# Kernel tuning notes

Measured on AMD Instinct MI355X. Metric: run time of the kernel, lower is better.

## Reference

```python
import jax, jax.numpy as jnp
import numpy as np

EMBED = 1024
HEADS = 16
HEAD_DIM = EMBED // HEADS


def setup_inputs() -> dict:
    key = jax.random.key(0)
    ks = jax.random.split(key, 5)
    s = 1.0 / np.sqrt(EMBED)
    x = jax.random.normal(ks[0], (2, 2048, EMBED), dtype=jnp.float32)
    W_qkv = jax.random.uniform(ks[1], (EMBED, 3 * EMBED), dtype=jnp.float32, minval=-s, maxval=s)
    b_qkv = jax.random.uniform(ks[2], (3 * EMBED,), dtype=jnp.float32, minval=-s, maxval=s)
    W_out = jax.random.uniform(ks[3], (EMBED, EMBED), dtype=jnp.float32, minval=-s, maxval=s)
    b_out = jax.random.uniform(ks[4], (EMBED,), dtype=jnp.float32, minval=-s, maxval=s)
    return {"x": x, "W_qkv": W_qkv, "b_qkv": b_qkv, "W_out": W_out, "b_out": b_out}


def reference(x, W_qkv, b_qkv, W_out, b_out):
    B, S, E = x.shape
    qkv = x @ W_qkv + b_qkv                              # [B,S,3E]
    qkv = qkv.reshape(B, S, 3, HEADS, HEAD_DIM)
    q, k, v = qkv[:, :, 0], qkv[:, :, 1], qkv[:, :, 2]   # [B,S,H,D]
    q = q.transpose(0, 2, 1, 3)                          # [B,H,S,D]
    k = k.transpose(0, 2, 1, 3)
    v = v.transpose(0, 2, 1, 3)
    scale = 1.0 / np.sqrt(HEAD_DIM).astype(np.float32)
    scores = jnp.einsum('bhqd,bhkd->bhqk', q, k) * scale  # [B,H,S,S]
    causal = jnp.tril(jnp.ones((S, S), dtype=bool))
    scores = jnp.where(causal, scores, jnp.float32(-jnp.inf))
    attn = jax.nn.softmax(scores, axis=-1)
    out = jnp.einsum('bhqk,bhkd->bhqd', attn, v)          # [B,H,S,D]
    out = out.transpose(0, 2, 1, 3).reshape(B, S, E)
    return out @ W_out + b_out
```

## Files before the change

kernel.cpp:

```cpp
#include <hip/hip_runtime.h>
#include <hip/hip_bf16.h>
#include <math.h>

typedef __bf16 bf16;
typedef bf16 bf16x4 __attribute__((ext_vector_type(4)));
typedef bf16 bf16x8 __attribute__((ext_vector_type(8)));
typedef float f32x4 __attribute__((ext_vector_type(4)));
typedef float f32x16 __attribute__((ext_vector_type(16)));
typedef unsigned int uint;

#define EMB 1024
#define SEQ 2048
#define BATCH 2
#define NH 16
#define HD 64

#define SCALE2 0.18033688011112042f

__device__ __forceinline__ void glds16(const void* g, void* l) {
  __builtin_amdgcn_global_load_lds(
      (__attribute__((address_space(1))) void*)g,
      (__attribute__((address_space(3))) void*)l, 16, 0, 0);
}

__device__ __forceinline__ uint cvtpk(float lo, float hi) {
  uint r;
  asm("v_cvt_pk_bf16_f32 %0, %1, %2" : "=v"(r) : "v"(lo), "v"(hi));
  return r;
}
__device__ __forceinline__ void plswap(uint& a, uint& b) {
  asm("v_permlane32_swap_b32 %0, %1" : "+v"(a), "+v"(b));
}

__global__ __launch_bounds__(256) void cvt_f32_bf16(const float* __restrict__ in,
                                                    bf16* __restrict__ out, int n) {
  int i = (blockIdx.x * 256 + threadIdx.x) * 4;
  if (i < n) {
    float4 v = *reinterpret_cast<const float4*>(in + i);
    out[i + 0] = (bf16)v.x;
    out[i + 1] = (bf16)v.y;
    out[i + 2] = (bf16)v.z;
    out[i + 3] = (bf16)v.w;
  }
}

__global__ __launch_bounds__(256) void transpose_cvt(const float* __restrict__ in,
                                                     bf16* __restrict__ out,
                                                     int R, int C) {
  __shared__ float tile[32][33];
  int c0 = blockIdx.x * 32, r0 = blockIdx.y * 32;
  int tx = threadIdx.x, ty = threadIdx.y;
#pragma unroll
  for (int i = 0; i < 32; i += 8)
    tile[ty + i][tx] = in[(size_t)(r0 + ty + i) * C + c0 + tx];
  __syncthreads();
#pragma unroll
  for (int i = 0; i < 32; i += 8)
    out[(size_t)(c0 + ty + i) * R + r0 + tx] = (bf16)tile[tx][ty + i];
}

#define BM 128
#define BN 128
#define BK 32

__global__ __launch_bounds__(256) void gemm_bf16(
    const bf16* __restrict__ A, const bf16* __restrict__ Bt,
    const float* __restrict__ bias, int M, int N, int K,
    float* __restrict__ outF,
    bf16* __restrict__ outQ, bf16* __restrict__ outK, bf16* __restrict__ outVt,
    int mode) {
  __shared__ bf16 Alds[BM][BK];
  __shared__ bf16 Blds[BN][BK];

  const int t = threadIdx.x;
  const int lane = t & 63;
  const int w = t >> 6;
  const int wr = w >> 1, wc = w & 1;
  const int lg = lane >> 4, lr = lane & 15;
  const int m0 = blockIdx.y * BM;
  const int n0 = blockIdx.x * BN;

  const int c0 = w * 64 + lane;
  const int c1 = 256 + w * 64 + lane;
  const int r0 = c0 >> 2, ch0 = c0 & 3;
  const int r1 = c1 >> 2, ch1 = c1 & 3;

  f32x4 acc[4][4] = {};

  for (int k0 = 0; k0 < K; k0 += BK) {
    __syncthreads();
    glds16(A + (size_t)(m0 + r0) * K + k0 + ch0 * 8, &Alds[0][0] + c0 * 8);
    glds16(A + (size_t)(m0 + r1) * K + k0 + ch1 * 8, &Alds[0][0] + c1 * 8);
    glds16(Bt + (size_t)(n0 + r0) * K + k0 + ch0 * 8, &Blds[0][0] + c0 * 8);
    glds16(Bt + (size_t)(n0 + r1) * K + k0 + ch1 * 8, &Blds[0][0] + c1 * 8);
    __syncthreads();

    bf16x8 af[4], bfr[4];
#pragma unroll
    for (int i = 0; i < 4; ++i)
      af[i] = *reinterpret_cast<const bf16x8*>(&Alds[wr * 64 + i * 16 + lr][lg * 8]);
#pragma unroll
    for (int j = 0; j < 4; ++j)
      bfr[j] = *reinterpret_cast<const bf16x8*>(&Blds[wc * 64 + j * 16 + lr][lg * 8]);
#pragma unroll
    for (int i = 0; i < 4; ++i)
#pragma unroll
      for (int j = 0; j < 4; ++j)
        acc[i][j] = __builtin_amdgcn_mfma_f32_16x16x32_bf16(af[i], bfr[j], acc[i][j], 0, 0, 0);
  }

#pragma unroll
  for (int j = 0; j < 4; ++j) {
    const int n = n0 + wc * 64 + j * 16 + lr;
    const float bi = bias[n];
#pragma unroll
    for (int i = 0; i < 4; ++i) {
      const int mb = m0 + wr * 64 + i * 16 + lg * 4;
      if (mode == 0) {
#pragma unroll
        for (int r = 0; r < 4; ++r)
          outF[(size_t)(mb + r) * N + n] = acc[i][j][r] + bi;
      } else {
        const int which = n >> 10, rem = n & 1023;
        const int hh = rem >> 6, d = rem & 63;
        const int bb = mb >> 11, ss = mb & 2047;
        if (which == 2) {
          bf16x4 pv;
#pragma unroll
          for (int r = 0; r < 4; ++r) pv[r] = (bf16)(acc[i][j][r] + bi);
          *reinterpret_cast<bf16x4*>(
              outVt + (((size_t)bb * NH + hh) * HD + d) * SEQ + ss) = pv;
        } else if (which == 0) {
          bf16* dst = outQ + (((size_t)bb * NH + hh) * SEQ + ss) * HD + d;
#pragma unroll
          for (int r = 0; r < 4; ++r)
            dst[(size_t)r * HD] = (bf16)((acc[i][j][r] + bi) * SCALE2);
        } else {
          bf16* dst = outK + (((size_t)bb * NH + hh) * SEQ + ss) * HD + d;
#pragma unroll
          for (int r = 0; r < 4; ++r) dst[(size_t)r * HD] = (bf16)(acc[i][j][r] + bi);
        }
      }
    }
  }
}


#define STAGE(kt_, buf_)                                                       \
  {                                                                            \
    const int kb_ = (kt_) << 6;                                                \
    _Pragma("unroll")                                                          \
    for (int j = 0; j < 4; ++j) {                                              \
      const int g = (j * 2 + w) * 64 + lane;                                   \
      const int row = g >> 3, cc = g & 7;                                      \
      const int pc = (cc ^ (row & 7)) << 3;                                    \
      glds16(Kb + headoff + (size_t)(kb_ + row) * HD + pc, &Kl[buf_][g * 8]);  \
      glds16(Vt + headoff + (size_t)row * SEQ + kb_ + pc, &Vl[buf_][g * 8]);   \
    }                                                                          \
  }

__global__ __launch_bounds__(128, 2) void attn_fwd(
    const bf16* __restrict__ Qb, const bf16* __restrict__ Kb,
    const bf16* __restrict__ Vt, bf16* __restrict__ Ob) {
  __shared__ bf16 Kl[2][64 * 64];
  __shared__ bf16 Vl[2][64 * 64];

  const int t = threadIdx.x;
  const int lane = t & 63;
  const int w = t >> 6;
  const int l31 = lane & 31;
  const int hi = lane >> 5;
  const int hi8 = hi << 3;
  const int swz = l31 & 7;

  const int id = blockIdx.x;
  const int qsup = 31 - (id >> 5);
  const int bh = id & 31;
  const int h = bh & 15, b = bh >> 4;
  const size_t headoff = ((size_t)b * NH + h) * SEQ * HD;
  const int qrow = qsup * 64 + w * 32 + l31;

  bf16x8 qf[4];
  {
    const bf16* qr = Qb + headoff + (size_t)qrow * HD + hi8;
#pragma unroll
    for (int d = 0; d < 4; ++d) qf[d] = *reinterpret_cast<const bf16x8*>(qr + d * 16);
  }

  f32x16 accO0 = {}, accO1 = {};
  float m = -1e30f, lsum = 0.f;
  const int nkt = qsup + 1;

  STAGE(0, 0);
  __syncthreads();

  for (int kt = 0; kt < nkt; ++kt) {
    const int cur = kt & 1;
    if (kt + 1 < nkt) STAGE(kt + 1, cur ^ 1);

    const int kb = kt << 6;
    f32x16 s0 = {}, s1 = {};
    __builtin_amdgcn_s_setprio(1);
#pragma unroll
    for (int dd = 0; dd < 4; ++dd) {
      const int pc = ((dd * 2 + hi) ^ swz) << 3;
      bf16x8 kf0 = *reinterpret_cast<const bf16x8*>(&Kl[cur][l31 * 64 + pc]);
      bf16x8 kf1 = *reinterpret_cast<const bf16x8*>(&Kl[cur][(l31 + 32) * 64 + pc]);
      s0 = __builtin_amdgcn_mfma_f32_32x32x16_bf16(kf0, qf[dd], s0, 0, 0, 0);
      s1 = __builtin_amdgcn_mfma_f32_32x32x16_bf16(kf1, qf[dd], s1, 0, 0, 0);
    }
    __builtin_amdgcn_s_setprio(0);
    if (kt == nkt - 1) {
      const int kq = kb + hi * 4 - qrow;
#pragma unroll
      for (int r = 0; r < 16; ++r) {
        const int off = (r & 3) + 8 * (r >> 2);
        if (kq + off > 0) s0[r] = -1e30f;
        if (kq + off + 32 > 0) s1[r] = -1e30f;
      }
    }
    float pm[16];
#pragma unroll
    for (int r = 0; r < 16; ++r) pm[r] = fmaxf(s0[r], s1[r]);
#pragma unroll
    for (int st = 8; st > 0; st >>= 1)
#pragma unroll
      for (int r = 0; r < st; ++r) pm[r] = fmaxf(pm[r], pm[r + st]);
    const float tm = fmaxf(pm[0], __shfl_xor(pm[0], 32));
    if (!__all(tm <= m + 8.f)) {
      const float newm = fmaxf(m, tm);
      const float corr = __builtin_amdgcn_exp2f(m - newm);
      m = newm;
      lsum *= corr;
      accO0 *= corr;
      accO1 *= corr;
    }
#pragma unroll
    for (int r = 0; r < 16; ++r) {
      s0[r] = __builtin_amdgcn_exp2f(s0[r] - m);
      s1[r] = __builtin_amdgcn_exp2f(s1[r] - m);
    }
    float ps[16];
#pragma unroll
    for (int r = 0; r < 16; ++r) ps[r] = s0[r] + s1[r];
#pragma unroll
    for (int st = 8; st > 0; st >>= 1)
#pragma unroll
      for (int r = 0; r < st; ++r) ps[r] += ps[r + st];
    lsum += ps[0] + __shfl_xor(ps[0], 32);
    uint wv[16];
    wv[0]  = cvtpk(s0[0],  s0[1]);  wv[1]  = cvtpk(s0[2],  s0[3]);
    wv[2]  = cvtpk(s0[4],  s0[5]);  wv[3]  = cvtpk(s0[6],  s0[7]);
    wv[4]  = cvtpk(s0[8],  s0[9]);  wv[5]  = cvtpk(s0[10], s0[11]);
    wv[6]  = cvtpk(s0[12], s0[13]); wv[7]  = cvtpk(s0[14], s0[15]);
    wv[8]  = cvtpk(s1[0],  s1[1]);  wv[9]  = cvtpk(s1[2],  s1[3]);
    wv[10] = cvtpk(s1[4],  s1[5]);  wv[11] = cvtpk(s1[6],  s1[7]);
    wv[12] = cvtpk(s1[8],  s1[9]);  wv[13] = cvtpk(s1[10], s1[11]);
    wv[14] = cvtpk(s1[12], s1[13]); wv[15] = cvtpk(s1[14], s1[15]);
    plswap(wv[0], wv[2]);   plswap(wv[1], wv[3]);
    plswap(wv[4], wv[6]);   plswap(wv[5], wv[7]);
    plswap(wv[8], wv[10]);  plswap(wv[9], wv[11]);
    plswap(wv[12], wv[14]); plswap(wv[13], wv[15]);
    __builtin_amdgcn_s_setprio(1);
#pragma unroll
    for (int ks = 0; ks < 4; ++ks) {
      uint4 u = make_uint4(wv[ks * 4], wv[ks * 4 + 1], wv[ks * 4 + 2], wv[ks * 4 + 3]);
      bf16x8 pf = *reinterpret_cast<bf16x8*>(&u);
      const int pc = ((ks * 2 + hi) ^ swz) << 3;
      bf16x8 vf0 = *reinterpret_cast<const bf16x8*>(&Vl[cur][l31 * 64 + pc]);
      bf16x8 vf1 = *reinterpret_cast<const bf16x8*>(&Vl[cur][(l31 + 32) * 64 + pc]);
      accO0 = __builtin_amdgcn_mfma_f32_32x32x16_bf16(vf0, pf, accO0, 0, 0, 0);
      accO1 = __builtin_amdgcn_mfma_f32_32x32x16_bf16(vf1, pf, accO1, 0, 0, 0);
    }
    __builtin_amdgcn_s_setprio(0);
    __syncthreads();
  }

  const float inv = 1.0f / lsum;
  bf16* orow = Ob + ((size_t)b * SEQ + qrow) * EMB + h * HD + hi * 4;
#pragma unroll
  for (int rq = 0; rq < 4; ++rq) {
    bf16x4 o0, o1;
#pragma unroll
    for (int i = 0; i < 4; ++i) {
      o0[i] = (bf16)(accO0[rq * 4 + i] * inv);
      o1[i] = (bf16)(accO1[rq * 4 + i] * inv);
    }
    *reinterpret_cast<bf16x4*>(orow + rq * 8) = o0;
    *reinterpret_cast<bf16x4*>(orow + 32 + rq * 8) = o1;
  }
}

extern "C" void kernel_launch(void* const* d_in, const int* in_sizes, int n_in,
                              void* d_out, int out_size, void* d_ws, size_t ws_size,
                              hipStream_t stream) {
  const float* x    = (const float*)d_in[0];
  const float* Wqkv = (const float*)d_in[1];
  const float* bqkv = (const float*)d_in[2];
  const float* Wout = (const float*)d_in[3];
  const float* bout = (const float*)d_in[4];
  float* out = (float*)d_out;

  char* ws = (char*)d_ws;
  bf16* xb     = (bf16*)(ws);
  bf16* wqkvt  = (bf16*)(ws + 8388608);
  bf16* woutt  = (bf16*)(ws + 14680064);
  bf16* Qb     = (bf16*)(ws + 16777216);
  bf16* Kb     = (bf16*)(ws + 25165824);
  bf16* Vtb    = (bf16*)(ws + 33554432);
  bf16* attnb  = (bf16*)(ws + 41943040);

  const int n1 = 4096 * 1024;
  cvt_f32_bf16<<<(n1 / 4 + 255) / 256, 256, 0, stream>>>(x, xb, n1);
  dim3 tb(32, 8);
  transpose_cvt<<<dim3(3072 / 32, 1024 / 32), tb, 0, stream>>>(Wqkv, wqkvt, 1024, 3072);
  transpose_cvt<<<dim3(1024 / 32, 1024 / 32), tb, 0, stream>>>(Wout, woutt, 1024, 1024);

  dim3 g1(3072 / BN, 4096 / BM);
  gemm_bf16<<<g1, 256, 0, stream>>>(xb, wqkvt, bqkv, 4096, 3072, 1024,
                                    nullptr, Qb, Kb, Vtb, 1);

  attn_fwd<<<1024, 128, 0, stream>>>(Qb, Kb, Vtb, attnb);

  dim3 g2(1024 / BN, 4096 / BM);
  gemm_bf16<<<g2, 256, 0, stream>>>(attnb, woutt, bout, 4096, 1024, 1024,
                                    out, nullptr, nullptr, nullptr, 0);
}
```

Measured before the change: 129.4 us.

## Enlarge attention tiles to 128 queries and 128 keys per block

The attention kernel moves from 64-query blocks of two waves to 128-query blocks of four waves. Each pipeline stage now brings in a 128-key K/V tile with a wider swizzle, so each staged tile serves twice as many query rows and block count and loop trips are halved. On the diagonal tile, QK and PV MFMAs for fully masked 32-key sub-tiles are skipped, and the block order is rearranged for the new 16 query blocks. The cost is many more live score registers (four 32x32 accumulators) and twice the LDS per block, which may reduce occupancy or cause spills.

```diff
diff --git a/kernel.cpp b/kernel.cpp
--- a/kernel.cpp
+++ b/kernel.cpp
@@ -148,22 +148,35 @@
 
 #define STAGE(kt_, buf_)                                                       \
   {                                                                            \
-    const int kb_ = (kt_) << 6;                                                \
+    const int kb_ = (kt_) << 7;                                                \
     _Pragma("unroll")                                                          \
     for (int j = 0; j < 4; ++j) {                                              \
-      const int g = (j * 2 + w) * 64 + lane;                                   \
-      const int row = g >> 3, cc = g & 7;                                      \
-      const int pc = (cc ^ (row & 7)) << 3;                                    \
-      glds16(Kb + headoff + (size_t)(kb_ + row) * HD + pc, &Kl[buf_][g * 8]);  \
-      glds16(Vt + headoff + (size_t)row * SEQ + kb_ + pc, &Vl[buf_][g * 8]);   \
+      const int g = j * 256 + t;                                               \
+      const int rowK = g >> 3, ccK = g & 7;                                    \
+      const int pcK = ((ccK ^ (rowK & 7)) << 3);                               \
+      glds16(Kb + headoff + (size_t)(kb_ + rowK) * HD + pcK, &Kl[buf_][g * 8]);\
+      const int rowV = g >> 4, ccV = g & 15;                                   \
+      const int pcV = ((ccV ^ (rowV & 15)) << 3);                              \
+      glds16(Vt + headoff + (size_t)rowV * SEQ + kb_ + pcV, &Vl[buf_][g * 8]); \
     }                                                                          \
   }
 
-__global__ __launch_bounds__(128, 2) void attn_fwd(
+#define QK_ACC(SX, X)                                                          \
+  if (!diag || (X) <= w) {                                                     \
+    _Pragma("unroll")                                                          \
+    for (int dd = 0; dd < 4; ++dd) {                                           \
+      const int pcK = (((dd * 2 + hi) ^ swzK) << 3);                           \
+      bf16x8 kf = *reinterpret_cast<const bf16x8*>(                            \
+          &Kl[cur][((X) * 32 + l31) * 64 + pcK]);                              \
+      SX = __builtin_amdgcn_mfma_f32_32x32x16_bf16(kf, qf[dd], SX, 0, 0, 0);   \
+    }                                                                          \
+  }
+
+__global__ __launch_bounds__(256, 2) void attn_fwd(
     const bf16* __restrict__ Qb, const bf16* __restrict__ Kb,
     const bf16* __restrict__ Vt, bf16* __restrict__ Ob) {
-  __shared__ bf16 Kl[2][64 * 64];
-  __shared__ bf16 Vl[2][64 * 64];
+  __shared__ bf16 Kl[2][128 * 64];
+  __shared__ bf16 Vl[2][64 * 128];
 
   const int t = threadIdx.x;
   const int lane = t & 63;
@@ -171,14 +184,15 @@
   const int l31 = lane & 31;
   const int hi = lane >> 5;
   const int hi8 = hi << 3;
-  const int swz = l31 & 7;
+  const int swzK = l31 & 7;
+  const int swzV = l31 & 15;
 
   const int id = blockIdx.x;
-  const int qsup = 31 - (id >> 5);
+  const int qb = (id < 256) ? (15 - (id >> 5)) : ((id - 256) >> 5);
   const int bh = id & 31;
   const int h = bh & 15, b = bh >> 4;
   const size_t headoff = ((size_t)b * NH + h) * SEQ * HD;
-  const int qrow = qsup * 64 + w * 32 + l31;
+  const int qrow = qb * 128 + w * 32 + l31;
 
   bf16x8 qf[4];
   {
@@ -189,7 +203,7 @@
 
   f32x16 accO0 = {}, accO1 = {};
   float m = -1e30f, lsum = 0.f;
-  const int nkt = qsup + 1;
+  const int nkt = qb + 1;
 
   STAGE(0, 0);
   __syncthreads();
@@ -198,30 +212,30 @@
     const int cur = kt & 1;
     if (kt + 1 < nkt) STAGE(kt + 1, cur ^ 1);
 
-    const int kb = kt << 6;
-    f32x16 s0 = {}, s1 = {};
+    const int kb = kt << 7;
+    const bool diag = (kt == nkt - 1);
+    f32x16 s0 = {}, s1 = {}, s2 = {}, s3 = {};
     __builtin_amdgcn_s_setprio(1);
-#pragma unroll
-    for (int dd = 0; dd < 4; ++dd) {
-      const int pc = ((dd * 2 + hi) ^ swz) << 3;
-      bf16x8 kf0 = *reinterpret_cast<const bf16x8*>(&Kl[cur][l31 * 64 + pc]);
-      bf16x8 kf1 = *reinterpret_cast<const bf16x8*>(&Kl[cur][(l31 + 32) * 64 + pc]);
-      s0 = __builtin_amdgcn_mfma_f32_32x32x16_bf16(kf0, qf[dd], s0, 0, 0, 0);
-      s1 = __builtin_amdgcn_mfma_f32_32x32x16_bf16(kf1, qf[dd], s1, 0, 0, 0);
-    }
+    QK_ACC(s0, 0)
+    QK_ACC(s1, 1)
+    QK_ACC(s2, 2)
+    QK_ACC(s3, 3)
     __builtin_amdgcn_s_setprio(0);
-    if (kt == nkt - 1) {
+    if (diag) {
       const int kq = kb + hi * 4 - qrow;
 #pragma unroll
       for (int r = 0; r < 16; ++r) {
         const int off = (r & 3) + 8 * (r >> 2);
         if (kq + off > 0) s0[r] = -1e30f;
         if (kq + off + 32 > 0) s1[r] = -1e30f;
+        if (kq + off + 64 > 0) s2[r] = -1e30f;
+        if (kq + off + 96 > 0) s3[r] = -1e30f;
       }
     }
     float pm[16];
 #pragma unroll
-    for (int r = 0; r < 16; ++r) pm[r] = fmaxf(s0[r], s1[r]);
+    for (int r = 0; r < 16; ++r)
+      pm[r] = fmaxf(fmaxf(s0[r], s1[r]), fmaxf(s2[r], s3[r]));
 #pragma unroll
     for (int st = 8; st > 0; st >>= 1)
 #pragma unroll
@@ -239,16 +253,19 @@
     for (int r = 0; r < 16; ++r) {
       s0[r] = __builtin_amdgcn_exp2f(s0[r] - m);
       s1[r] = __builtin_amdgcn_exp2f(s1[r] - m);
+      s2[r] = __builtin_amdgcn_exp2f(s2[r] - m);
+      s3[r] = __builtin_amdgcn_exp2f(s3[r] - m);
     }
     float ps[16];
 #pragma unroll
-    for (int r = 0; r < 16; ++r) ps[r] = s0[r] + s1[r];
+    for (int r = 0; r < 16; ++r)
+      ps[r] = (s0[r] + s1[r]) + (s2[r] + s3[r]);
 #pragma unroll
     for (int st = 8; st > 0; st >>= 1)
 #pragma unroll
       for (int r = 0; r < st; ++r) ps[r] += ps[r + st];
     lsum += ps[0] + __shfl_xor(ps[0], 32);
-    uint wv[16];
+    uint wv[32];
     wv[0]  = cvtpk(s0[0],  s0[1]);  wv[1]  = cvtpk(s0[2],  s0[3]);
     wv[2]  = cvtpk(s0[4],  s0[5]);  wv[3]  = cvtpk(s0[6],  s0[7]);
     wv[4]  = cvtpk(s0[8],  s0[9]);  wv[5]  = cvtpk(s0[10], s0[11]);
@@ -257,20 +274,38 @@
     wv[10] = cvtpk(s1[4],  s1[5]);  wv[11] = cvtpk(s1[6],  s1[7]);
     wv[12] = cvtpk(s1[8],  s1[9]);  wv[13] = cvtpk(s1[10], s1[11]);
     wv[14] = cvtpk(s1[12], s1[13]); wv[15] = cvtpk(s1[14], s1[15]);
+    wv[16] = cvtpk(s2[0],  s2[1]);  wv[17] = cvtpk(s2[2],  s2[3]);
+    wv[18] = cvtpk(s2[4],  s2[5]);  wv[19] = cvtpk(s2[6],  s2[7]);
+    wv[20] = cvtpk(s2[8],  s2[9]);  wv[21] = cvtpk(s2[10], s2[11]);
+    wv[22] = cvtpk(s2[12], s2[13]); wv[23] = cvtpk(s2[14], s2[15]);
+    wv[24] = cvtpk(s3[0],  s3[1]);  wv[25] = cvtpk(s3[2],  s3[3]);
+    wv[26] = cvtpk(s3[4],  s3[5]);  wv[27] = cvtpk(s3[8],  s3[9]);
+    wv[27] = cvtpk(s3[6],  s3[7]);  wv[28] = cvtpk(s3[8],  s3[9]);
+    wv[29] = cvtpk(s3[10], s3[11]);
+    wv[30] = cvtpk(s3[12], s3[13]); wv[31] = cvtpk(s3[14], s3[15]);
     plswap(wv[0], wv[2]);   plswap(wv[1], wv[3]);
     plswap(wv[4], wv[6]);   plswap(wv[5], wv[7]);
     plswap(wv[8], wv[10]);  plswap(wv[9], wv[11]);
     plswap(wv[12], wv[14]); plswap(wv[13], wv[15]);
+    plswap(wv[16], wv[18]); plswap(wv[17], wv[19]);
+    plswap(wv[20], wv[22]); plswap(wv[21], wv[23]);
+    plswap(wv[24], wv[26]); plswap(wv[25], wv[27]);
+    plswap(wv[28], wv[30]); plswap(wv[29], wv[31]);
     __builtin_amdgcn_s_setprio(1);
 #pragma unroll
-    for (int ks = 0; ks < 4; ++ks) {
-      uint4 u = make_uint4(wv[ks * 4], wv[ks * 4 + 1], wv[ks * 4 + 2], wv[ks * 4 + 3]);
-      bf16x8 pf = *reinterpret_cast<bf16x8*>(&u);
-      const int pc = ((ks * 2 + hi) ^ swz) << 3;
-      bf16x8 vf0 = *reinterpret_cast<const bf16x8*>(&Vl[cur][l31 * 64 + pc]);
-      bf16x8 vf1 = *reinterpret_cast<const bf16x8*>(&Vl[cur][(l31 + 32) * 64 + pc]);
-      accO0 = __builtin_amdgcn_mfma_f32_32x32x16_bf16(vf0, pf, accO0, 0, 0, 0);
-      accO1 = __builtin_amdgcn_mfma_f32_32x32x16_bf16(vf1, pf, accO1, 0, 0, 0);
+    for (int ks = 0; ks < 8; ++ks) {
+      if (!diag || ks < 2 * w + 2) {
+        uint4 u = make_uint4(wv[(ks >> 1) * 8 + (ks & 1) * 4],
+                             wv[(ks >> 1) * 8 + (ks & 1) * 4 + 1],
+                             wv[(ks >> 1) * 8 + (ks & 1) * 4 + 2],
+                             wv[(ks >> 1) * 8 + (ks & 1) * 4 + 3]);
+        bf16x8 pf = *reinterpret_cast<bf16x8*>(&u);
+        const int pcV = (((ks * 2 + hi) ^ swzV) << 3);
+        bf16x8 vf0 = *reinterpret_cast<const bf16x8*>(&Vl[cur][l31 * 128 + pcV]);
+        bf16x8 vf1 = *reinterpret_cast<const bf16x8*>(&Vl[cur][(l31 + 32) * 128 + pcV]);
+        accO0 = __builtin_amdgcn_mfma_f32_32x32x16_bf16(vf0, pf, accO0, 0, 0, 0);
+        accO1 = __builtin_amdgcn_mfma_f32_32x32x16_bf16(vf1, pf, accO1, 0, 0, 0);
+      }
     }
     __builtin_amdgcn_s_setprio(0);
     __syncthreads();
@@ -320,7 +355,7 @@
   gemm_bf16<<<g1, 256, 0, stream>>>(xb, wqkvt, bqkv, 4096, 3072, 1024,
                                     nullptr, Qb, Kb, Vtb, 1);
 
-  attn_fwd<<<1024, 128, 0, stream>>>(Qb, Kb, Vtb, attnb);
+  attn_fwd<<<512, 256, 0, stream>>>(Qb, Kb, Vtb, attnb);
 
   dim3 g2(1024 / BN, 4096 / BM);
   gemm_bf16<<<g2, 256, 0, stream>>>(attnb, woutt, bout, 4096, 1024, 1024,
```

After: 125.2 us. 1.03x faster.
